# Kernel optimization log

Measured on AMD Instinct MI355X. Metric: run time of the kernel, lower is better.

The kernel has to match this reference:

```python
import jax, jax.numpy as jnp
import numpy as np


def _shift(w):
    # max(0, -min(w)): scalar shift making w + shift non-negative
    return jnp.maximum(0.0, -jnp.min(w))


def shifted_linear(x, W, b=None):
    # F.linear with non-negative weights plus row-sum correction
    alpha = _shift(W)
    y = x @ (W + alpha).T - alpha * jnp.sum(x, axis=-1, keepdims=True)
    if b is not None:
        y = y + b
    return y


def shifted_depthwise_conv(x, w, b):
    # x: (B, D, L), w: (D, 1, K) depthwise; causal-style padding K-1, sliced to L by caller
    alpha = _shift(w)
    k = w.shape[2]
    pad = k - 1
    dn = ('NCH', 'OIH', 'NCH')
    groups = w.shape[0]
    y = jax.lax.conv_general_dilated(x, w + alpha, (1,), [(pad, pad)],
                                     dimension_numbers=dn, feature_group_count=groups)
    ones_k = jnp.ones_like(w)
    ssum = jax.lax.conv_general_dilated(x, ones_k, (1,), [(pad, pad)],
                                        dimension_numbers=dn, feature_group_count=groups)
    return y - alpha * ssum + b[None, :, None]


def setup_inputs() -> dict:
    key = jax.random.key(0)
    ks = jax.random.split(key, 10)
    d_model, d_inner, d_state, d_conv, dt_rank = 1024, 2048, 16, 4, 64
    B, L = 2, 1024
    s = 0.05
    return {
        'hidden_states': jax.random.normal(ks[0], (B, L, d_model), jnp.float32),
        'W_in': jax.random.normal(ks[1], (2 * d_inner, d_model), jnp.float32) * s,
        'conv_w': jax.random.normal(ks[2], (d_inner, 1, d_conv), jnp.float32) * 0.3,
        'conv_b': jax.random.normal(ks[3], (d_inner,), jnp.float32) * s,
        'W_x': jax.random.normal(ks[4], (dt_rank + 2 * d_state, d_inner), jnp.float32) * s,
        'W_dt': jax.random.normal(ks[5], (d_inner, dt_rank), jnp.float32) * s,
        'dt_bias': jax.random.normal(ks[6], (d_inner,), jnp.float32),
        'W_out': jax.random.normal(ks[7], (d_model, d_inner), jnp.float32) * s,
        'A_log': jax.random.normal(ks[8], (d_inner, d_state), jnp.float32) * 0.5,
        'D': jax.random.normal(ks[9], (d_inner,), jnp.float32),
    }


def reference(hidden_states, W_in, conv_w, conv_b, W_x, W_dt, dt_bias, W_out, A_log, D):
    b, l, dm = hidden_states.shape
    d_inner = conv_w.shape[0]
    d_state = A_log.shape[1]
    dt_rank = W_dt.shape[1]

    A = jnp.exp(A_log)  # (d_inner, d_state), always positive

    # in_proj over (b*l, d_model) -> (b, 2*d_inner, l)
    xz = shifted_linear(hidden_states.reshape(b * l, dm), W_in)
    xz = xz.reshape(b, l, 2 * d_inner).transpose(0, 2, 1)
    x, z = xz[:, :d_inner], xz[:, d_inner:]

    # depthwise shifted conv + SiLU activation, truncated to seqlen
    x = jax.nn.silu(shifted_depthwise_conv(x, conv_w, conv_b)[..., :l])

    # x_proj -> dt_raw, B, C
    x_dbl = shifted_linear(x.transpose(0, 2, 1).reshape(b * l, d_inner), W_x)
    dt_raw = x_dbl[:, :dt_rank]
    Bm = x_dbl[:, dt_rank:dt_rank + d_state].reshape(b, l, d_state).transpose(0, 2, 1)  # (b,n,l)
    Cm = x_dbl[:, dt_rank + d_state:].reshape(b, l, d_state).transpose(0, 2, 1)         # (b,n,l)
    dt = shifted_linear(dt_raw, W_dt).reshape(b, l, d_inner).transpose(0, 2, 1)          # (b,d,l)

    # delta activation (softplus) with bias, clamped
    delta = jnp.clip(jax.nn.softplus(dt + dt_bias[None, :, None]), 1e-4, 20.0)

    # global scalar shifts for B and C
    beta = _shift(Bm)
    gamma = _shift(Cm)
    B_nn = Bm + beta
    C_nn = Cm + gamma

    # precomputed per-step operands, scan axis first: (l, b, d, n)
    deltaA = jnp.exp(-jnp.einsum('bdl,dn->lbdn', delta, A))
    dBu = jnp.einsum('bdl,bnl,bdl->lbdn', delta, B_nn, x)
    C_scan = C_nn.transpose(2, 0, 1)  # (l, b, n)

    def step(xc, inp):
        dA_i, dBu_i, C_i = inp
        xc = dA_i * xc + dBu_i                                   # (b,d,n)
        y = jnp.einsum('bdn,bn->bd', xc, C_i) - gamma * jnp.sum(xc, axis=-1)
        return xc, y

    x0 = jnp.zeros((b, d_inner, d_state), dtype=delta.dtype)
    _, ys = jax.lax.scan(step, x0, (deltaA, dBu, C_scan))        # ys: (l, b, d)

    y = ys.transpose(1, 2, 0) + x * D[None, :, None]             # (b, d, l) skip term
    y = y * jax.nn.silu(z)                                       # gate activation

    out = shifted_linear(y.transpose(0, 2, 1).reshape(b * l, d_inner), W_out)
    return out.reshape(b, l, dm)
```

## Files before the change

### kernel.cpp

```cpp
#include <hip/hip_runtime.h>
#include <math.h>

#define DM 1024
#define DI 2048
#define DS 16
#define DTR 64
#define NB 2
#define LL 1024
#define TT (NB*LL)
#define SCH 32
#define NCH (LL/SCH)

typedef unsigned short u16;
typedef __attribute__((ext_vector_type(8))) short bf16x8;
typedef __attribute__((ext_vector_type(4))) float f32x4;

#define LOG2E 1.4426950408889634f
#define LN2   0.6931471805599453f

__device__ inline u16 f2bf(float f) {
  union { float f; unsigned u; } c; c.f = f;
  unsigned u = c.u;
  return (u16)((u + 0x7fffu + ((u >> 16) & 1u)) >> 16);
}
__device__ inline float bf2f(u16 u) {
  union { unsigned u; float f; } c; c.u = ((unsigned)u) << 16;
  return c.f;
}

__device__ inline float fsilu(float x) {
  return x * __builtin_amdgcn_rcpf(1.0f + __builtin_amdgcn_exp2f(-x * LOG2E));
}

__device__ inline unsigned fkey(float f) {
  union { float f; unsigned u; } c; c.f = f;
  return (c.u & 0x80000000u) ? ~c.u : (c.u | 0x80000000u);
}
__device__ inline float funkey(unsigned k) {
  union { unsigned u; float f; } c;
  c.u = (k & 0x80000000u) ? (k & 0x7fffffffu) : ~k;
  return c.f;
}

__device__ inline bf16x8 cvt8(float4 a, float4 b) {
  bf16x8 w;
  w[0] = (short)f2bf(a.x); w[1] = (short)f2bf(a.y);
  w[2] = (short)f2bf(a.z); w[3] = (short)f2bf(a.w);
  w[4] = (short)f2bf(b.x); w[5] = (short)f2bf(b.y);
  w[6] = (short)f2bf(b.z); w[7] = (short)f2bf(b.w);
  return w;
}

#define GLDS16(g, l) __builtin_amdgcn_global_load_lds( \
    (const __attribute__((address_space(1))) unsigned int*)(g), \
    (__attribute__((address_space(3))) unsigned int*)(l), 16, 0, 0)

template<int BM, int BN, int EPI, int OB, int CGd, int ASRC, int BMIN>
__global__ __launch_bounds__(256) void gemm_k(
    const void* __restrict__ Av, const u16* __restrict__ B,
    void* __restrict__ Cv, int M, int N, int K, int lda, int ldb, int kpb,
    const float* __restrict__ bias,
    const float* __restrict__ minsrc, unsigned* __restrict__ betakey) {
  constexpr int WAVES_M = BM / 64;
  constexpr int WAVES_N = 4 / WAVES_M;
  constexpr int WTM = 4;
  constexpr int WTN = BN / (WAVES_N * 16);
  constexpr int ASLABS = BM / 16;
  constexpr int SLABS = (BM + BN) / 16;
  constexpr int SPW = SLABS / 4;
  __shared__ u16 As[2][BM * 32];
  __shared__ u16 Bs[2][BN * 32];
  __shared__ float sm4[4];
  const int tid = threadIdx.x;
  const int wave = tid >> 6;
  const int lane = tid & 63;
  const int bm = blockIdx.y * BM;
  const int bn = blockIdx.x * BN;
  const int wm = (wave / WAVES_N) * 64;
  const int wn = (wave % WAVES_N) * (WTN * 16);
  const int r4 = lane >> 2;
  const int kc = (lane & 3) * 8;
  const int fr = lane & 15;
  const int fq = lane >> 4;
  const int koff = blockIdx.z * kpb;
  float* C = (float*)Cv;
  u16* C16 = (u16*)Cv;

  if constexpr (BMIN == 1) {
    int fb = blockIdx.y * gridDim.x + blockIdx.x;
    if (fb < 64) {
      const int t0 = fb * 32;
      float mn = 3.4e38f;
      for (int i = tid; i < 32 * 16; i += 256) {
        int t = t0 + (i >> 4), n = i & 15;
        mn = fminf(mn, minsrc[t * 96 + 64 + n]);
      }
#pragma unroll
      for (int o = 32; o; o >>= 1) mn = fminf(mn, __shfl_down(mn, o));
      if ((tid & 63) == 0) sm4[tid >> 6] = mn;
      __syncthreads();
      if (tid == 0)
        atomicMin(betakey, fkey(fminf(fminf(sm4[0], sm4[1]), fminf(sm4[2], sm4[3]))));
      __syncthreads();
    }
  }

  auto stage = [&](int k0, int bufi) {
#pragma unroll
    for (int s = wave * SPW; s < (wave + 1) * SPW; ++s) {
      if (s < ASLABS) {
        int row = s * 16 + r4;
        if constexpr (ASRC == 0) {
          GLDS16((const u16*)Av + (size_t)(bm + row) * lda + k0 + kc,
                 &As[bufi][s * 512]);
        } else {
          const float* src = (const float*)Av + (size_t)(bm + row) * lda + k0 + kc;
          float4 v0 = *(const float4*)src;
          float4 v1 = *(const float4*)(src + 4);
          *(bf16x8*)&As[bufi][s * 512 + lane * 8] = cvt8(v0, v1);
        }
      } else {
        int bs = s - ASLABS;
        int row = bs * 16 + r4;
        GLDS16(B + (size_t)(bn + row) * ldb + k0 + kc, &Bs[bufi][bs * 512]);
      }
    }
  };

  f32x4 acc[WTM][WTN];
#pragma unroll
  for (int i = 0; i < WTM; ++i)
#pragma unroll
    for (int j = 0; j < WTN; ++j) acc[i][j] = (f32x4){0.f, 0.f, 0.f, 0.f};

  const int NT = kpb >> 5;
  stage(koff, 0);
  asm volatile("s_waitcnt vmcnt(0) lgkmcnt(0)" ::: "memory");
  __builtin_amdgcn_s_barrier();
  for (int t = 0; t < NT; ++t) {
    const int cur = t & 1;
    if (t + 1 < NT) stage(koff + (t + 1) * 32, cur ^ 1);
    bf16x8 af[WTM], bf[WTN];
#pragma unroll
    for (int i = 0; i < WTM; ++i)
      af[i] = *(const bf16x8*)&As[cur][(wm + 16 * i + fr) * 32 + fq * 8];
#pragma unroll
    for (int j = 0; j < WTN; ++j)
      bf[j] = *(const bf16x8*)&Bs[cur][(wn + 16 * j + fr) * 32 + fq * 8];
#pragma unroll
    for (int i = 0; i < WTM; ++i)
#pragma unroll
      for (int j = 0; j < WTN; ++j)
        acc[i][j] = __builtin_amdgcn_mfma_f32_16x16x32_bf16(af[i], bf[j], acc[i][j], 0, 0, 0);
    if (t + 1 < NT) {
      asm volatile("s_waitcnt vmcnt(0) lgkmcnt(0)" ::: "memory");
      __builtin_amdgcn_s_barrier();
    }
  }

#pragma unroll
  for (int i = 0; i < WTM; ++i) {
    int row0 = bm + wm + 16 * i + fq * 4;
#pragma unroll
    for (int j = 0; j < WTN; ++j) {
      int col = bn + wn + 16 * j + fr;
#pragma unroll
      for (int r = 0; r < 4; ++r) {
        float v = acc[i][j][r];
        if (EPI == 1) {
          v += bias[col];
          float sp;
          if (v > 20.0f) sp = v;
          else sp = __builtin_amdgcn_logf(1.0f + __builtin_amdgcn_exp2f(v * LOG2E)) * LN2;
          v = fminf(fmaxf(sp, 1e-4f), 20.0f);
        }
        if (OB == 1) {
          C16[(size_t)(row0 + r) * N + col] = f2bf(v);
        } else {
          if (CGd == 0 || col < CGd) {
            const int ldc = (CGd > 0) ? CGd : N;
            atomicAdd(&C[(size_t)(row0 + r) * ldc + col], v);
          }
        }
      }
    }
  }
}

__global__ __launch_bounds__(256) void cast_all(
    const float* __restrict__ hs, const float* __restrict__ win,
    const float* __restrict__ wout, const float* __restrict__ wx,
    const float* __restrict__ wdt,
    u16* __restrict__ hs_bf, u16* __restrict__ win_bf,
    u16* __restrict__ wout_bf, u16* __restrict__ wx_bf,
    u16* __restrict__ wdt_bf, float* __restrict__ xdb,
    float* __restrict__ outz, unsigned* __restrict__ betakey) {
  int gid = blockIdx.x * 256 + threadIdx.x;
  if (gid == 0) betakey[0] = 0xFFFFFFFFu;
  const float* src; u16* dst; int off;
  if (gid < 524288)       { src = hs;   dst = hs_bf;   off = gid; }
  else if (gid < 1572864) { src = win;  dst = win_bf;  off = gid - 524288; }
  else if (gid < 2097152) { src = wout; dst = wout_bf; off = gid - 1572864; }
  else if (gid < 2146304) { src = wx;   dst = wx_bf;   off = gid - 2097152; }
  else if (gid < 2179072) { src = wdt;  dst = wdt_bf;  off = gid - 2146304; }
  else if (gid < 2195456) {
    ushort4 z4 = {0, 0, 0, 0};
    ((ushort4*)wx_bf)[49152 + gid - 2179072] = z4;
    return;
  } else if (gid < 2244608) {
    float4 z = {0.f, 0.f, 0.f, 0.f};
    ((float4*)xdb)[gid - 2195456] = z;
    return;
  } else {
    float4 z = {0.f, 0.f, 0.f, 0.f};
    ((float4*)outz)[gid - 2244608] = z;
    return;
  }
  float4 v = ((const float4*)src)[off];
  ushort4 o;
  o.x = f2bf(v.x); o.y = f2bf(v.y); o.z = f2bf(v.z); o.w = f2bf(v.w);
  ((ushort4*)dst)[off] = o;
}

__global__ __launch_bounds__(256) void conv_silu4(
    const u16* __restrict__ xz, const float* __restrict__ w,
    const float* __restrict__ cb, u16* __restrict__ xc_bf) {
  int gid = blockIdx.x * 256 + threadIdx.x;
  int dq = (gid & 511) * 4;
  int t = gid >> 9;
  int l = t & (LL - 1);
  float wv[4][4];
#pragma unroll
  for (int j = 0; j < 4; ++j) {
    float4 ww = *(const float4*)&w[(dq + j) * 4];
    wv[j][0] = ww.x; wv[j][1] = ww.y; wv[j][2] = ww.z; wv[j][3] = ww.w;
  }
  float4 acc = *(const float4*)&cb[dq];
#pragma unroll
  for (int k = 0; k < 4; ++k) {
    int ll = l - 3 + k;
    if (ll < 0) continue;
    ushort4 xv = *(const ushort4*)&xz[(size_t)(t - 3 + k) * (2 * DI) + dq];
    acc.x += bf2f(xv.x) * wv[0][k]; acc.y += bf2f(xv.y) * wv[1][k];
    acc.z += bf2f(xv.z) * wv[2][k]; acc.w += bf2f(xv.w) * wv[3][k];
  }
  acc.x = fsilu(acc.x); acc.y = fsilu(acc.y);
  acc.z = fsilu(acc.z); acc.w = fsilu(acc.w);
  ushort4 o;
  o.x = f2bf(acc.x); o.y = f2bf(acc.y); o.z = f2bf(acc.z); o.w = f2bf(acc.w);
  *(ushort4*)&xc_bf[(size_t)t * DI + dq] = o;
}

__global__ __launch_bounds__(256) void scan_pass1(
    const u16* __restrict__ delta, const u16* __restrict__ xc_bf,
    const float* __restrict__ xdb, const float* __restrict__ A_log,
    const unsigned* __restrict__ betak,
    float* __restrict__ hend, float* __restrict__ Ssum) {
  const int d = blockIdx.x * 256 + threadIdx.x;
  const int c = blockIdx.y;
  const int b = blockIdx.z;
  __shared__ float Bsh[SCH][16];
  const float beta = fmaxf(0.0f, -funkey(betak[0]));
  const int t0 = b * LL + c * SCH;
  for (int i = threadIdx.x; i < SCH * 16; i += 256) {
    int tt = i >> 4, n = i & 15;
    Bsh[tt][n] = xdb[(size_t)(t0 + tt) * 96 + 64 + n] + beta;
  }
  __syncthreads();
  float Av2[16];
#pragma unroll
  for (int n = 0; n < 16; ++n)
    Av2[n] = __builtin_amdgcn_exp2f(A_log[d * 16 + n] * LOG2E) * LOG2E;
  float h[16];
#pragma unroll
  for (int n = 0; n < 16; ++n) h[n] = 0.f;
  float S = 0.f;
  for (int tt = 0; tt < SCH; ++tt) {
    int t = t0 + tt;
    float dv = bf2f(delta[(size_t)t * DI + d]);
    float xv = bf2f(xc_bf[(size_t)t * DI + d]);
    float dx = dv * xv;
    S += dv;
#pragma unroll
    for (int n = 0; n < 16; ++n) {
      float a = __builtin_amdgcn_exp2f(-dv * Av2[n]);
      h[n] = a * h[n] + dx * Bsh[tt][n];
    }
  }
  size_t base = (((size_t)(b * NCH + c) * DI) + d) * 16;
#pragma unroll
  for (int n = 0; n < 16; ++n) hend[base + n] = h[n];
  Ssum[((size_t)(b * NCH + c) * DI) + d] = S;
}

__global__ __launch_bounds__(256) void scan_pass2(
    float* __restrict__ hend, const float* __restrict__ Ssum,
    const float* __restrict__ A_log) {
  int gid = blockIdx.x * 256 + threadIdx.x;
  int n = gid & 15;
  int d = (gid >> 4) & (DI - 1);
  int b = gid >> 15;
  float Av2 = __builtin_amdgcn_exp2f(A_log[d * 16 + n] * LOG2E) * LOG2E;
  float H = 0.f;
  for (int c = 0; c < NCH; ++c) {
    size_t cb = ((size_t)(b * NCH + c) * DI) + d;
    float hl = hend[cb * 16 + n];
    float p = __builtin_amdgcn_exp2f(-Av2 * Ssum[cb]);
    hend[cb * 16 + n] = H;
    H = p * H + hl;
  }
}

__global__ __launch_bounds__(256) void scan_pass3(
    const u16* __restrict__ delta, const u16* __restrict__ xc_bf,
    const float* __restrict__ xdb, const u16* __restrict__ xz_bf,
    const float* __restrict__ A_log, const float* __restrict__ Dp,
    const unsigned* __restrict__ betak, const float* __restrict__ hstart,
    u16* __restrict__ ybf) {
  const int d = blockIdx.x * 256 + threadIdx.x;
  const int c = blockIdx.y;
  const int b = blockIdx.z;
  __shared__ float Bsh[SCH][16];
  __shared__ float Csh[SCH][16];
  const float beta = fmaxf(0.0f, -funkey(betak[0]));
  const int t0 = b * LL + c * SCH;
  for (int i = threadIdx.x; i < SCH * 16; i += 256) {
    int tt = i >> 4, n = i & 15;
    size_t row = (size_t)(t0 + tt) * 96;
    Bsh[tt][n] = xdb[row + 64 + n] + beta;
    Csh[tt][n] = xdb[row + 80 + n];
  }
  __syncthreads();
  float Av2[16];
#pragma unroll
  for (int n = 0; n < 16; ++n)
    Av2[n] = __builtin_amdgcn_exp2f(A_log[d * 16 + n] * LOG2E) * LOG2E;
  float h[16];
  size_t base = (((size_t)(b * NCH + c) * DI) + d) * 16;
#pragma unroll
  for (int n = 0; n < 16; ++n) h[n] = hstart[base + n];
  const float Dd = Dp[d];
  for (int tt = 0; tt < SCH; ++tt) {
    int t = t0 + tt;
    float dv = bf2f(delta[(size_t)t * DI + d]);
    float xv = bf2f(xc_bf[(size_t)t * DI + d]);
    float dx = dv * xv;
    float yv = 0.f;
#pragma unroll
    for (int n = 0; n < 16; ++n) {
      float a = __builtin_amdgcn_exp2f(-dv * Av2[n]);
      h[n] = a * h[n] + dx * Bsh[tt][n];
      yv += h[n] * Csh[tt][n];
    }
    float zv = bf2f(xz_bf[(size_t)t * (2 * DI) + DI + d]);
    float out = (yv + xv * Dd) * fsilu(zv);
    ybf[(size_t)t * DI + d] = f2bf(out);
  }
}

extern "C" void kernel_launch(void* const* d_in, const int* in_sizes, int n_in,
                              void* d_out, int out_size, void* d_ws, size_t ws_size,
                              hipStream_t stream) {
  const float* hs      = (const float*)d_in[0];
  const float* W_in    = (const float*)d_in[1];
  const float* conv_w  = (const float*)d_in[2];
  const float* conv_b  = (const float*)d_in[3];
  const float* W_x     = (const float*)d_in[4];
  const float* W_dt    = (const float*)d_in[5];
  const float* dt_bias = (const float*)d_in[6];
  const float* W_out   = (const float*)d_in[7];
  const float* A_log   = (const float*)d_in[8];
  const float* Dp      = (const float*)d_in[9];
  float* out = (float*)d_out;

  float* ws       = (float*)d_ws;
  float* xz_bfR   = ws;
  float* xcv_bfR  = xz_bfR + (size_t)TT * 2 * DI / 2;
  float* xdb      = xcv_bfR + (size_t)TT * DI / 2;
  float* dlt_bfR  = xdb + (size_t)TT * 96;
  float* betab    = dlt_bfR + (size_t)TT * DI / 2;
  float* hend     = betab + 64;
  float* Ssum     = hend + (size_t)NB * NCH * DI * 16;
  float* hs_bfR   = Ssum + (size_t)NB * NCH * DI;
  float* win_bfR  = hs_bfR + (size_t)TT * DM / 2;
  float* wout_bfR = win_bfR + (size_t)2 * DI * DM / 2;
  float* wx_bfR   = wout_bfR + (size_t)DM * DI / 2;
  float* wdt_bfR  = wx_bfR + 131072;

  u16* xz_bf   = (u16*)xz_bfR;
  u16* xcv_bf  = (u16*)xcv_bfR;
  u16* dlt_bf  = (u16*)dlt_bfR;
  u16* hs_bf   = (u16*)hs_bfR;
  u16* win_bf  = (u16*)win_bfR;
  u16* wout_bf = (u16*)wout_bfR;
  u16* wx_bf   = (u16*)wx_bfR;
  u16* wdt_bf  = (u16*)wdt_bfR;
  unsigned* betakey = (unsigned*)betab;
  u16* ybf     = (u16*)win_bfR;

  dim3 blk(256);

  cast_all<<<10816, blk, 0, stream>>>(hs, W_in, W_out, W_x, W_dt,
                                      hs_bf, win_bf, wout_bf, wx_bf, wdt_bf,
                                      xdb, out, betakey);

  gemm_k<128, 128, 0, 1, 0, 0, 0>
      <<<dim3(4096 / 128, TT / 128), blk, 0, stream>>>(
      hs_bf, win_bf, xz_bf, TT, 2 * DI, DM, DM, DM, DM,
      nullptr, nullptr, nullptr);

  conv_silu4<<<(TT * DI / 4) / 256, blk, 0, stream>>>(xz_bf, conv_w, conv_b, xcv_bf);

  gemm_k<64, 128, 0, 2, 96, 0, 0>
      <<<dim3(1, TT / 64, 8), blk, 0, stream>>>(
      xcv_bf, wx_bf, xdb, TT, 128, DI, DI, DI, DI / 8,
      nullptr, nullptr, nullptr);

  gemm_k<64, 128, 1, 1, 0, 1, 1>
      <<<dim3(DI / 128, TT / 64), blk, 0, stream>>>(
      xdb, wdt_bf, dlt_bf, TT, DI, DTR, 96, DTR, DTR,
      dt_bias, xdb, betakey);

  scan_pass1<<<dim3(DI / 256, NCH, NB), blk, 0, stream>>>(
      dlt_bf, xcv_bf, xdb, A_log, betakey, hend, Ssum);
  scan_pass2<<<(NB * DI * DS) / 256, blk, 0, stream>>>(hend, Ssum, A_log);
  scan_pass3<<<dim3(DI / 256, NCH, NB), blk, 0, stream>>>(
      dlt_bf, xcv_bf, xdb, xz_bf, A_log, Dp, betakey, hend, ybf);

  gemm_k<128, 128, 0, 2, 0, 0, 0>
      <<<dim3(DM / 128, TT / 128, 4), blk, 0, stream>>>(
      ybf, wout_bf, out, TT, DM, DI, DI, DI, DI / 4,
      nullptr, nullptr, nullptr);
}
```

Measured before the change: 239.0 us.

## Fuse causal conv+SiLU into x_proj GEMM A-load and triple-buffer big GEMMs

Removes the standalone depthwise conv+SiLU kernel. The x_proj GEMM now computes conv and SiLU on the fly while staging A tiles from xz, and also writes xcv out for the scan. Separately, the in_proj and out_proj GEMMs gain a three-buffer LDS pipeline with partial vmcnt waits so loads run two tiles ahead. This saves a launch and one round trip of xcv through memory, at the cost of redundant xz reads across the 4 taps inside the GEMM and more LDS per block.

```diff
diff --git a/kernel.cpp b/kernel.cpp
--- a/kernel.cpp
+++ b/kernel.cpp
@@ -55,12 +55,14 @@
     (const __attribute__((address_space(1))) unsigned int*)(g), \
     (__attribute__((address_space(3))) unsigned int*)(l), 16, 0, 0)
 
-template<int BM, int BN, int EPI, int OB, int CGd, int ASRC, int BMIN>
+template<int BM, int BN, int EPI, int OB, int CGd, int ASRC, int BMIN, int PIPE3>
 __global__ __launch_bounds__(256) void gemm_k(
     const void* __restrict__ Av, const u16* __restrict__ B,
     void* __restrict__ Cv, int M, int N, int K, int lda, int ldb, int kpb,
     const float* __restrict__ bias,
-    const float* __restrict__ minsrc, unsigned* __restrict__ betakey) {
+    const float* __restrict__ minsrc, unsigned* __restrict__ betakey,
+    const float* __restrict__ cw, const float* __restrict__ cbias,
+    u16* __restrict__ xcv_out) {
   constexpr int WAVES_M = BM / 64;
   constexpr int WAVES_N = 4 / WAVES_M;
   constexpr int WTM = 4;
@@ -68,8 +70,10 @@
   constexpr int ASLABS = BM / 16;
   constexpr int SLABS = (BM + BN) / 16;
   constexpr int SPW = SLABS / 4;
-  __shared__ u16 As[2][BM * 32];
-  __shared__ u16 Bs[2][BN * 32];
+  constexpr int NBUF = PIPE3 ? 3 : 2;
+  static_assert(!PIPE3 || (ASRC == 0 && SPW == 4), "PIPE3 needs ASRC=0, SPW=4");
+  __shared__ u16 As[NBUF][BM * 32];
+  __shared__ u16 Bs[NBUF][BN * 32];
   __shared__ float sm4[4];
   const int tid = threadIdx.x;
   const int wave = tid >> 6;
@@ -113,11 +117,33 @@
         if constexpr (ASRC == 0) {
           GLDS16((const u16*)Av + (size_t)(bm + row) * lda + k0 + kc,
                  &As[bufi][s * 512]);
-        } else {
+        } else if constexpr (ASRC == 1) {
           const float* src = (const float*)Av + (size_t)(bm + row) * lda + k0 + kc;
           float4 v0 = *(const float4*)src;
           float4 v1 = *(const float4*)(src + 4);
           *(bf16x8*)&As[bufi][s * 512 + lane * 8] = cvt8(v0, v1);
+        } else {
+          int t = bm + row;
+          int l = t & (LL - 1);
+          int dq = k0 + kc;
+          const u16* xzp = (const u16*)Av;
+          float a0[8];
+#pragma unroll
+          for (int j = 0; j < 8; ++j) a0[j] = cbias[dq + j];
+#pragma unroll
+          for (int k = 0; k < 4; ++k) {
+            int ll = l - 3 + k;
+            if (ll < 0) continue;
+            bf16x8 xv = *(const bf16x8*)&xzp[(size_t)(t - 3 + k) * (2 * DI) + dq];
+#pragma unroll
+            for (int j = 0; j < 8; ++j)
+              a0[j] += bf2f((u16)xv[j]) * cw[(dq + j) * 4 + k];
+          }
+          bf16x8 w8;
+#pragma unroll
+          for (int j = 0; j < 8; ++j) w8[j] = (short)f2bf(fsilu(a0[j]));
+          *(bf16x8*)&As[bufi][s * 512 + lane * 8] = w8;
+          *(bf16x8*)&xcv_out[(size_t)t * DI + dq] = w8;
         }
       } else {
         int bs = s - ASLABS;
@@ -134,12 +160,8 @@
     for (int j = 0; j < WTN; ++j) acc[i][j] = (f32x4){0.f, 0.f, 0.f, 0.f};
 
   const int NT = kpb >> 5;
-  stage(koff, 0);
-  asm volatile("s_waitcnt vmcnt(0) lgkmcnt(0)" ::: "memory");
-  __builtin_amdgcn_s_barrier();
-  for (int t = 0; t < NT; ++t) {
-    const int cur = t & 1;
-    if (t + 1 < NT) stage(koff + (t + 1) * 32, cur ^ 1);
+
+  auto compute = [&](int cur) {
     bf16x8 af[WTM], bf[WTN];
 #pragma unroll
     for (int i = 0; i < WTM; ++i)
@@ -152,9 +174,35 @@
 #pragma unroll
       for (int j = 0; j < WTN; ++j)
         acc[i][j] = __builtin_amdgcn_mfma_f32_16x16x32_bf16(af[i], bf[j], acc[i][j], 0, 0, 0);
-    if (t + 1 < NT) {
-      asm volatile("s_waitcnt vmcnt(0) lgkmcnt(0)" ::: "memory");
-      __builtin_amdgcn_s_barrier();
+  };
+
+  if constexpr (PIPE3) {
+    stage(koff, 0);
+    stage(koff + 32, 1);
+    asm volatile("s_waitcnt vmcnt(4)" ::: "memory");
+    __builtin_amdgcn_s_barrier();
+    for (int t = 0; t < NT; ++t) {
+      const int cur = t % 3;
+      if (t + 2 < NT) stage(koff + (t + 2) * 32, (t + 2) % 3);
+      compute(cur);
+      if (t + 1 < NT) {
+        if (t + 2 < NT) asm volatile("s_waitcnt vmcnt(4)" ::: "memory");
+        else            asm volatile("s_waitcnt vmcnt(0)" ::: "memory");
+        __builtin_amdgcn_s_barrier();
+      }
+    }
+  } else {
+    stage(koff, 0);
+    asm volatile("s_waitcnt vmcnt(0) lgkmcnt(0)" ::: "memory");
+    __builtin_amdgcn_s_barrier();
+    for (int t = 0; t < NT; ++t) {
+      const int cur = t & 1;
+      if (t + 1 < NT) stage(koff + (t + 1) * 32, cur ^ 1);
+      compute(cur);
+      if (t + 1 < NT) {
+        asm volatile("s_waitcnt vmcnt(0) lgkmcnt(0)" ::: "memory");
+        __builtin_amdgcn_s_barrier();
+      }
     }
   }
 
@@ -222,35 +270,6 @@
   ((ushort4*)dst)[off] = o;
 }
 
-__global__ __launch_bounds__(256) void conv_silu4(
-    const u16* __restrict__ xz, const float* __restrict__ w,
-    const float* __restrict__ cb, u16* __restrict__ xc_bf) {
-  int gid = blockIdx.x * 256 + threadIdx.x;
-  int dq = (gid & 511) * 4;
-  int t = gid >> 9;
-  int l = t & (LL - 1);
-  float wv[4][4];
-#pragma unroll
-  for (int j = 0; j < 4; ++j) {
-    float4 ww = *(const float4*)&w[(dq + j) * 4];
-    wv[j][0] = ww.x; wv[j][1] = ww.y; wv[j][2] = ww.z; wv[j][3] = ww.w;
-  }
-  float4 acc = *(const float4*)&cb[dq];
-#pragma unroll
-  for (int k = 0; k < 4; ++k) {
-    int ll = l - 3 + k;
-    if (ll < 0) continue;
-    ushort4 xv = *(const ushort4*)&xz[(size_t)(t - 3 + k) * (2 * DI) + dq];
-    acc.x += bf2f(xv.x) * wv[0][k]; acc.y += bf2f(xv.y) * wv[1][k];
-    acc.z += bf2f(xv.z) * wv[2][k]; acc.w += bf2f(xv.w) * wv[3][k];
-  }
-  acc.x = fsilu(acc.x); acc.y = fsilu(acc.y);
-  acc.z = fsilu(acc.z); acc.w = fsilu(acc.w);
-  ushort4 o;
-  o.x = f2bf(acc.x); o.y = f2bf(acc.y); o.z = f2bf(acc.z); o.w = f2bf(acc.w);
-  *(ushort4*)&xc_bf[(size_t)t * DI + dq] = o;
-}
-
 __global__ __launch_bounds__(256) void scan_pass1(
     const u16* __restrict__ delta, const u16* __restrict__ xc_bf,
     const float* __restrict__ xdb, const float* __restrict__ A_log,
@@ -404,22 +423,20 @@
                                       hs_bf, win_bf, wout_bf, wx_bf, wdt_bf,
                                       xdb, out, betakey);
 
-  gemm_k<128, 128, 0, 1, 0, 0, 0>
+  gemm_k<128, 128, 0, 1, 0, 0, 0, 1>
       <<<dim3(4096 / 128, TT / 128), blk, 0, stream>>>(
       hs_bf, win_bf, xz_bf, TT, 2 * DI, DM, DM, DM, DM,
-      nullptr, nullptr, nullptr);
-
-  conv_silu4<<<(TT * DI / 4) / 256, blk, 0, stream>>>(xz_bf, conv_w, conv_b, xcv_bf);
-
-  gemm_k<64, 128, 0, 2, 96, 0, 0>
+      nullptr, nullptr, nullptr, nullptr, nullptr, nullptr);
+
+  gemm_k<64, 128, 0, 2, 96, 2, 0, 0>
       <<<dim3(1, TT / 64, 8), blk, 0, stream>>>(
-      xcv_bf, wx_bf, xdb, TT, 128, DI, DI, DI, DI / 8,
-      nullptr, nullptr, nullptr);
-
-  gemm_k<64, 128, 1, 1, 0, 1, 1>
+      xz_bf, wx_bf, xdb, TT, 128, DI, 2 * DI, DI, DI / 8,
+      nullptr, nullptr, nullptr, conv_w, conv_b, xcv_bf);
+
+  gemm_k<64, 128, 1, 1, 0, 1, 1, 0>
       <<<dim3(DI / 128, TT / 64), blk, 0, stream>>>(
       xdb, wdt_bf, dlt_bf, TT, DI, DTR, 96, DTR, DTR,
-      dt_bias, xdb, betakey);
+      dt_bias, xdb, betakey, nullptr, nullptr, nullptr);
 
   scan_pass1<<<dim3(DI / 256, NCH, NB), blk, 0, stream>>>(
       dlt_bf, xcv_bf, xdb, A_log, betakey, hend, Ssum);
@@ -427,8 +444,8 @@
   scan_pass3<<<dim3(DI / 256, NCH, NB), blk, 0, stream>>>(
       dlt_bf, xcv_bf, xdb, xz_bf, A_log, Dp, betakey, hend, ybf);
 
-  gemm_k<128, 128, 0, 2, 0, 0, 0>
+  gemm_k<128, 128, 0, 2, 0, 0, 0, 1>
       <<<dim3(DM / 128, TT / 128, 4), blk, 0, stream>>>(
       ybf, wout_bf, out, TT, DM, DI, DI, DI, DI / 4,
-      nullptr, nullptr, nullptr);
-}
+      nullptr, nullptr, nullptr, nullptr, nullptr, nullptr);
+}
```

Measured after the change: 243.8 us. Within noise of the previous version (+2.0%).
